# Kernel tuning notes

Measured on AMD Instinct MI355X. Metric: run time of the kernel, lower is better.

Reference implementation:

```python
import jax, jax.numpy as jnp
import numpy as np

B, S, C, H, E, K = 8, 512, 768, 12, 8, 2
MLP_H = int(C * 4.0)
HD = C // H
ROUTER_REG = 0.01
LN_EPS = 1e-5


def setup_inputs() -> dict:
    key = jax.random.key(0)
    ks = jax.random.split(key, 8)

    def w(k, shape, fan_in):
        return (jax.random.normal(k, shape, dtype=jnp.float32) / np.sqrt(fan_in)).astype(jnp.float32)

    return {
        "x": jax.random.normal(ks[0], (B, S, C), dtype=jnp.float32),
        "expert_tokens": w(ks[1], (E, C), C),
        "ln1_g": jnp.ones((E, C), jnp.float32),
        "ln1_b": jnp.zeros((E, C), jnp.float32),
        "qkv_w": w(ks[2], (E, C, 3 * C), C),
        "qkv_b": jnp.zeros((E, 3 * C), jnp.float32),
        "proj_w": w(ks[3], (E, C, C), C),
        "proj_b": jnp.zeros((E, C), jnp.float32),
        "ln2_g": jnp.ones((E, C), jnp.float32),
        "ln2_b": jnp.zeros((E, C), jnp.float32),
        "fc1_w": w(ks[4], (E, C, MLP_H), C),
        "fc1_b": jnp.zeros((E, MLP_H), jnp.float32),
        "fc2_w": w(ks[5], (E, MLP_H, C), MLP_H),
        "fc2_b": jnp.zeros((E, C), jnp.float32),
    }


def _layernorm(x, g, b):
    mu = jnp.mean(x, axis=-1, keepdims=True)
    var = jnp.mean(jnp.square(x - mu), axis=-1, keepdims=True)
    return (x - mu) * jax.lax.rsqrt(var + LN_EPS) * g + b


def _block(x, p):
    # One transformer Block (pre-LN attention + MLP), params for a single expert.
    ln1_g, ln1_b, qkv_w, qkv_b, proj_w, proj_b, ln2_g, ln2_b, fc1_w, fc1_b, fc2_w, fc2_b = p
    h = _layernorm(x, ln1_g, ln1_b)
    qkv = (h @ qkv_w + qkv_b).reshape(B, S, 3, H, HD)
    q, k, v = qkv[:, :, 0], qkv[:, :, 1], qkv[:, :, 2]  # [B,S,H,HD]
    # NOTE: original code MULTIPLIES by sqrt(head_dim) (scale = head_dim**0.5).
    scale = jnp.float32(np.sqrt(HD))
    attn = jax.nn.softmax(jnp.einsum('bqhd,bkhd->bhqk', q, k) * scale, axis=-1)
    o = jnp.einsum('bhqk,bkhd->bqhd', attn, v).reshape(B, S, C)
    x = x + (o @ proj_w + proj_b)
    h2 = _layernorm(x, ln2_g, ln2_b)
    x = x + (jax.nn.gelu(h2 @ fc1_w + fc1_b, approximate=False) @ fc2_w + fc2_b)
    return x


def reference(x, expert_tokens, ln1_g, ln1_b, qkv_w, qkv_b, proj_w, proj_b,
              ln2_g, ln2_b, fc1_w, fc1_b, fc2_w, fc2_b):
    # Router
    router_logits = jnp.einsum('bsc,nc->bsn', x, expert_tokens) / jnp.float32(np.sqrt(C))
    router_probs = jax.nn.softmax(router_logits, axis=-1)
    top_k_probs, top_k_idx = jax.lax.top_k(router_probs, K)  # [B,S,K]
    top_k_probs = top_k_probs / jnp.sum(top_k_probs, axis=-1, keepdims=True)

    # Dense all-expert compute (sequential over experts to bound memory)
    params = (ln1_g, ln1_b, qkv_w, qkv_b, proj_w, proj_b, ln2_g, ln2_b,
              fc1_w, fc1_b, fc2_w, fc2_b)
    expert_out = jax.lax.map(lambda p: _block(x, p), params)  # [E,B,S,C]
    expert_out = jnp.transpose(expert_out, (1, 2, 0, 3))       # [B,S,E,C]

    # Top-k gather and weighted combine
    sel = jnp.take_along_axis(expert_out, top_k_idx[..., None], axis=2)  # [B,S,K,C]
    combine = jnp.sum(sel * top_k_probs[..., None], axis=2)
    out = x + combine

    # Load-balance auxiliary loss
    counts = jnp.sum(jax.nn.one_hot(top_k_idx, E, dtype=jnp.float32), axis=(0, 1, 2))
    f_i = counts / jnp.float32(B * S * K)
    P_i = jnp.mean(router_probs, axis=(0, 1))
    balance_loss = E * jnp.sum(f_i * P_i) + ROUTER_REG * jnp.linalg.norm(expert_tokens)
    return out, balance_loss
```

## Files before the change

### kernel.cpp

```cpp
#include <hip/hip_runtime.h>
#include <hip/hip_bf16.h>

#define BB 8
#define SS 512
#define CC 768
#define HH 12
#define HD 64
#define EE 8
#define KK 2
#define MLPH 3072
#define NT (BB*SS)
#define NOUT (NT*CC)

#define SLOTB      68059136ull
#define SLOT_U16   34029568ull
#define SLOT_F32   17014784ull

typedef unsigned int u32;
typedef unsigned short u16;
typedef __attribute__((ext_vector_type(8))) short short8;
typedef __attribute__((ext_vector_type(4))) float f32x4;

__device__ __forceinline__ u16 f2bf(float f) {
    u32 u = __builtin_bit_cast(u32, f);
    u32 r = (u + 0x7fffu + ((u >> 16) & 1u)) >> 16;
    return (u16)r;
}
__device__ __forceinline__ float bf2f(u16 h) {
    u32 u = ((u32)h) << 16;
    return __builtin_bit_cast(float, u);
}
__device__ __forceinline__ void gl_lds16(const void* g, void* l) {
    __builtin_amdgcn_global_load_lds(
        (const __attribute__((address_space(1))) u32*)g,
        (__attribute__((address_space(3))) u32*)l, 16, 0, 0);
}
__device__ __forceinline__ void swz_rc(int bid, int& bm, int& bn) {
    int xcd = bid & 7, off = bid >> 3;
    bm = (xcd * 4 + (off & 3)) * 128;
    bn = (off >> 2) * 128;
}

__device__ __forceinline__ void stage128x64(const u16* __restrict__ G, size_t ldg,
                                            u16* s, int tid)
{
    int wid = tid >> 6, lane = tid & 63;
#pragma unroll
    for (int it = 0; it < 4; ++it) {
        int cb = it * 256 + wid * 64;
        int c = cb + lane;
        int row = c >> 3;
        int ch = (c & 7) ^ (row & 7);
        gl_lds16(G + (size_t)row * ldg + ch * 8, s + cb * 8);
    }
}
__device__ __forceinline__ short8 frag64(const u16* s, int row, int kc, int lb) {
    int ch = (kc * 4 + lb) ^ (row & 7);
    return *(const short8*)(s + row * 64 + ch * 8);
}

__global__ __launch_bounds__(256) void router_kernel(const float* __restrict__ x,
    const float* __restrict__ et, float* __restrict__ W, float* __restrict__ stats)
{
    __shared__ float etl[EE * CC];
    __shared__ float pred[4][2 * EE];
    int tid = threadIdx.x;
    for (int i = tid; i < EE * CC; i += 256) etl[i] = et[i];
    __syncthreads();
    int wid = tid >> 6, lane = tid & 63;
    float psum[EE] = {}, csum[EE] = {};
    for (int i = 0; i < 2; i++) {
        int t = blockIdx.x * 8 + wid * 2 + i;
        const float* xr = x + (size_t)t * CC;
        float acc[EE] = {};
        for (int c = lane; c < CC; c += 64) {
            float xv = xr[c];
#pragma unroll
            for (int e = 0; e < EE; e++) acc[e] += xv * etl[e * CC + c];
        }
#pragma unroll
        for (int e = 0; e < EE; e++)
            for (int off = 1; off < 64; off <<= 1) acc[e] += __shfl_xor(acc[e], off, 64);
        if (lane == 0) {
            const float inv = 0.03608439182435161f;
            float l[EE], m = -1e30f;
#pragma unroll
            for (int e = 0; e < EE; e++) { l[e] = acc[e] * inv; m = fmaxf(m, l[e]); }
            float p[EE], sum = 0.f;
#pragma unroll
            for (int e = 0; e < EE; e++) { p[e] = __expf(l[e] - m); sum += p[e]; }
            int i1 = 0;
#pragma unroll
            for (int e = 1; e < EE; e++) if (p[e] > p[i1]) i1 = e;
            int i2 = -1;
#pragma unroll
            for (int e = 0; e < EE; e++) if (e != i1 && (i2 < 0 || p[e] > p[i2])) i2 = e;
            float wn = p[i1] + p[i2];
#pragma unroll
            for (int e = 0; e < EE; e++) W[t * EE + e] = 0.f;
            W[t * EE + i1] = p[i1] / wn;
            W[t * EE + i2] = p[i2] / wn;
#pragma unroll
            for (int e = 0; e < EE; e++) psum[e] += p[e] / sum;
            csum[i1] += 1.f; csum[i2] += 1.f;
        }
    }
    if (lane == 0) {
#pragma unroll
        for (int e = 0; e < EE; e++) { pred[wid][e] = psum[e]; pred[wid][EE + e] = csum[e]; }
    }
    __syncthreads();
    if (tid < 2 * EE) {
        float s = pred[0][tid] + pred[1][tid] + pred[2][tid] + pred[3][tid];
        atomicAdd(&stats[tid], s);
    }
}

template<int MODE>
__global__ __launch_bounds__(256) void ln_kernel(const float* __restrict__ x, size_t xslot,
    u16* __restrict__ out_hi, u16* __restrict__ out_lo, size_t oslot)
{
    int t = blockIdx.x;
    int eb = blockIdx.y;
    const float* xr = x + (size_t)eb * xslot + (size_t)t * CC;
    __shared__ float red[256];
    int tid = threadIdx.x;
    float v[3];
    float s = 0.f;
#pragma unroll
    for (int i = 0; i < 3; i++) { v[i] = xr[tid + i * 256]; s += v[i]; }
    red[tid] = s; __syncthreads();
    for (int off = 128; off > 0; off >>= 1) { if (tid < off) red[tid] += red[tid + off]; __syncthreads(); }
    float mu = red[0] / (float)CC;
    __syncthreads();
    float s2 = 0.f;
#pragma unroll
    for (int i = 0; i < 3; i++) { float d = v[i] - mu; s2 += d * d; }
    red[tid] = s2; __syncthreads();
    for (int off = 128; off > 0; off >>= 1) { if (tid < off) red[tid] += red[tid + off]; __syncthreads(); }
    float var = red[0] / (float)CC;
    float sc = rsqrtf(var + 1e-5f);
#pragma unroll
    for (int i = 0; i < 3; i++) {
        int c = tid + i * 256;
        float val = (v[i] - mu) * sc;
        u16 hi = f2bf(val);
        out_hi[(size_t)eb * oslot + (size_t)t * CC + c] = hi;
        if (MODE) out_lo[(size_t)eb * oslot + (size_t)t * CC + c] = f2bf(val - bf2f(hi));
    }
}

__global__ __launch_bounds__(256) void prep_expert(
    const float* __restrict__ qkv_w0, const float* __restrict__ qkv_b0,
    const float* __restrict__ proj_w0,
    const float* __restrict__ fc1_w0, const float* __restrict__ fc1_b0,
    const float* __restrict__ fc2_w0,
    const float* __restrict__ g1_0, const float* __restrict__ b1_0,
    const float* __restrict__ g2_0, const float* __restrict__ b2_0,
    u16* __restrict__ qkvTh, u16* __restrict__ qkvTl,
    u16* __restrict__ projT, u16* __restrict__ fc1T, u16* __restrict__ fc2T,
    float* __restrict__ biasq, float* __restrict__ biasf1, int ebase)
{
    __shared__ float tile[32][33];
    __shared__ float bsh[CC];
    __shared__ float redg[256];
    int bid = blockIdx.x;
    int eb = blockIdx.y;
    int ge = ebase + eb;
    int tid = threadIdx.x;
    const float* qkv_w = qkv_w0 + (size_t)ge * CC * 3 * CC;
    const float* qkv_b = qkv_b0 + (size_t)ge * 3 * CC;
    const float* proj_w = proj_w0 + (size_t)ge * CC * CC;
    const float* fc1_w = fc1_w0 + (size_t)ge * CC * MLPH;
    const float* fc1_b = fc1_b0 + (size_t)ge * MLPH;
    const float* fc2_w = fc2_w0 + (size_t)ge * MLPH * CC;
    const float* g1 = g1_0 + (size_t)ge * CC;
    const float* b1 = b1_0 + (size_t)ge * CC;
    const float* g2 = g2_0 + (size_t)ge * CC;
    const float* b2 = b2_0 + (size_t)ge * CC;

    if (bid < 6912) {
        const float* src; const float* scale = nullptr;
        u16 *dh, *dl = nullptr; int N, Kd, n0, k0;
        if (bid < 1728) {
            src = qkv_w; scale = g1;
            dh = qkvTh + (size_t)eb * SLOT_U16; dl = qkvTl + (size_t)eb * SLOT_U16;
            N = 2304; Kd = 768; n0 = (bid % 72) * 32; k0 = (bid / 72) * 32;
        } else if (bid < 2304) {
            int i = bid - 1728;
            src = proj_w; dh = projT + (size_t)eb * SLOT_U16; N = 768; Kd = 768;
            n0 = (i % 24) * 32; k0 = (i / 24) * 32;
        } else if (bid < 4608) {
            int i = bid - 2304;
            src = fc1_w; scale = g2; dh = fc1T + (size_t)eb * SLOT_U16; N = 3072; Kd = 768;
            n0 = (i % 96) * 32; k0 = (i / 96) * 32;
        } else {
            int i = bid - 4608;
            src = fc2_w; dh = fc2T + (size_t)eb * SLOT_U16; N = 768; Kd = 3072;
            n0 = (i % 24) * 32; k0 = (i / 24) * 32;
        }
        int tx = tid & 31, ty = tid >> 5;
#pragma unroll
        for (int i = 0; i < 32; i += 8) {
            float v = src[(size_t)(k0 + ty + i) * N + n0 + tx];
            if (scale) v *= scale[k0 + ty + i];
            tile[ty + i][tx] = v;
        }
        __syncthreads();
#pragma unroll
        for (int i = 0; i < 32; i += 8) {
            float v = tile[tx][ty + i];
            u16 hi = f2bf(v);
            dh[(size_t)(n0 + ty + i) * Kd + k0 + tx] = hi;
            if (dl) dl[(size_t)(n0 + ty + i) * Kd + k0 + tx] = f2bf(v - bf2f(hi));
        }
    } else {
        const float* bv; const float* wsrc; const float* badd;
        float* dst; int N, n0;
        if (bid < 6984) { bv = b1; wsrc = qkv_w; badd = qkv_b; dst = biasq + (size_t)eb * SLOT_F32; N = 2304; n0 = (bid - 6912) * 32; }
        else            { bv = b2; wsrc = fc1_w; badd = fc1_b; dst = biasf1 + (size_t)eb * SLOT_F32; N = MLPH; n0 = (bid - 6984) * 32; }
        for (int i = tid; i < CC; i += 256) bsh[i] = bv[i];
        __syncthreads();
        int g = tid & 31, l8 = tid >> 5;
        int n = n0 + g;
        float acc = 0.f;
        for (int k = l8; k < CC; k += 8) acc += bsh[k] * wsrc[(size_t)k * N + n];
        redg[tid] = acc; __syncthreads();
        if (tid < 32) {
            float sum = 0.f;
#pragma unroll
            for (int i = 0; i < 8; i++) sum += redg[tid + i * 32];
            dst[n0 + tid] = sum + badd[n0 + tid];
        }
    }
}

__global__ __launch_bounds__(256) void gemm_qkv_bk64(
    const u16* __restrict__ Ah, const u16* __restrict__ Al,
    const u16* __restrict__ Bh0, const u16* __restrict__ Bl0,
    const float* __restrict__ biasq0, u16* __restrict__ qk_hi0,
    u16* __restrict__ qk_lo0, u16* __restrict__ vtout0)
{
    __shared__ __align__(16) u16 sAh[128 * 64], sAl[128 * 64];
    __shared__ __align__(16) u16 sBh[128 * 64], sBl[128 * 64];
    int tid = threadIdx.x;
    int eb = blockIdx.y;
    int bm, bn;
    swz_rc(blockIdx.x, bm, bn);
    bool qk_tile = (bn < 1536);
    int wid = tid >> 6, lane = tid & 63;
    int wr = wid >> 1, wc = wid & 1;
    int la = lane & 15, lb = lane >> 4;
    const u16* Bh = Bh0 + (size_t)eb * SLOT_U16;
    const u16* Bl = Bl0 + (size_t)eb * SLOT_U16;
    const float* bias = biasq0 + (size_t)eb * SLOT_F32;
    u16* qk_hi = qk_hi0 + (size_t)eb * SLOT_U16;
    u16* qk_lo = qk_lo0 + (size_t)eb * SLOT_U16;
    u16* vtout = vtout0 + (size_t)eb * SLOT_U16;

    f32x4 acc[4][4];
#pragma unroll
    for (int i = 0; i < 4; i++)
#pragma unroll
        for (int j = 0; j < 4; j++) acc[i][j] = (f32x4){0.f, 0.f, 0.f, 0.f};

    const u16* Abh = Ah + (size_t)bm * CC;
    const u16* Abl = Al + (size_t)bm * CC;
    const u16* Bbh = Bh + (size_t)bn * CC;
    const u16* Bbl = Bl + (size_t)bn * CC;
    for (int k0 = 0; k0 < CC; k0 += 64) {
        stage128x64(Abh + k0, CC, sAh, tid);
        stage128x64(Bbh + k0, CC, sBh, tid);
        if (qk_tile) {
            stage128x64(Abl + k0, CC, sAl, tid);
            stage128x64(Bbl + k0, CC, sBl, tid);
        }
        __syncthreads();
        if (qk_tile) {
#pragma unroll
            for (int kc = 0; kc < 2; kc++) {
                short8 avh[4], avl[4], bvh[4], bvl[4];
#pragma unroll
                for (int i = 0; i < 4; i++) {
                    int row = wr * 64 + i * 16 + la;
                    avh[i] = frag64(sAh, row, kc, lb);
                    avl[i] = frag64(sAl, row, kc, lb);
                }
#pragma unroll
                for (int j = 0; j < 4; j++) {
                    int row = wc * 64 + j * 16 + la;
                    bvh[j] = frag64(sBh, row, kc, lb);
                    bvl[j] = frag64(sBl, row, kc, lb);
                }
#pragma unroll
                for (int i = 0; i < 4; i++)
#pragma unroll
                    for (int j = 0; j < 4; j++) {
                        acc[i][j] = __builtin_amdgcn_mfma_f32_16x16x32_bf16(avh[i], bvh[j], acc[i][j], 0, 0, 0);
                        acc[i][j] = __builtin_amdgcn_mfma_f32_16x16x32_bf16(avh[i], bvl[j], acc[i][j], 0, 0, 0);
                        acc[i][j] = __builtin_amdgcn_mfma_f32_16x16x32_bf16(avl[i], bvh[j], acc[i][j], 0, 0, 0);
                    }
            }
        } else {
#pragma unroll
            for (int kc = 0; kc < 2; kc++) {
                short8 avh[4], bvh[4];
#pragma unroll
                for (int i = 0; i < 4; i++) avh[i] = frag64(sAh, wr * 64 + i * 16 + la, kc, lb);
#pragma unroll
                for (int j = 0; j < 4; j++) bvh[j] = frag64(sBh, wc * 64 + j * 16 + la, kc, lb);
#pragma unroll
                for (int i = 0; i < 4; i++)
#pragma unroll
                    for (int j = 0; j < 4; j++)
                        acc[i][j] = __builtin_amdgcn_mfma_f32_16x16x32_bf16(avh[i], bvh[j], acc[i][j], 0, 0, 0);
            }
        }
        __syncthreads();
    }
#pragma unroll
    for (int i = 0; i < 4; i++) {
#pragma unroll
        for (int j = 0; j < 4; j++) {
            int gn = bn + wc * 64 + j * 16 + la;
            float bsv = bias[gn];
#pragma unroll
            for (int r = 0; r < 4; r++) {
                int gm = bm + wr * 64 + i * 16 + lb * 4 + r;
                float v = acc[i][j][r] + bsv;
                if (gn < 1536) {
                    u16 hi = f2bf(v);
                    qk_hi[(size_t)gm * 1536 + gn] = hi;
                    qk_lo[(size_t)gm * 1536 + gn] = f2bf(v - bf2f(hi));
                } else {
                    int dd = (gn - 1536) & 63, hh = (gn - 1536) >> 6;
                    int ss = gm & (SS - 1), bb = gm >> 9;
                    vtout[((size_t)((bb * HH + hh) * HD + dd)) * SS + ss] = f2bf(v);
                }
            }
        }
    }
}

template<int EPI>
__global__ __launch_bounds__(256) void gemm_b(
    const u16* __restrict__ A, size_t Aslot,
    const u16* __restrict__ BT, size_t Bslot,
    const float* __restrict__ bias, size_t biasSlot,
    const float* __restrict__ res, size_t resSlot,
    const float* __restrict__ Wt, int ebase,
    const float* __restrict__ xinit,
    void* __restrict__ Cout, size_t CoutSlot, int N, int Kdim)
{
    __shared__ __align__(16) u16 sA[128 * 64];
    __shared__ __align__(16) u16 sB[128 * 64];
    int tid = threadIdx.x;
    int eb = blockIdx.y;
    int ge = ebase + eb;
    int bm, bn;
    swz_rc(blockIdx.x, bm, bn);
    int wid = tid >> 6, lane = tid & 63;
    int wr = wid >> 1, wc = wid & 1;
    int la = lane & 15, lb = lane >> 4;
    f32x4 acc[4][4];
#pragma unroll
    for (int i = 0; i < 4; i++)
#pragma unroll
        for (int j = 0; j < 4; j++) acc[i][j] = (f32x4){0.f, 0.f, 0.f, 0.f};

    const u16* Ab = A + (size_t)eb * Aslot + (size_t)bm * Kdim;
    const u16* Bb = BT + (size_t)eb * Bslot + (size_t)bn * Kdim;
    for (int k0 = 0; k0 < Kdim; k0 += 64) {
        stage128x64(Ab + k0, Kdim, sA, tid);
        stage128x64(Bb + k0, Kdim, sB, tid);
        __syncthreads();
#pragma unroll
        for (int kc = 0; kc < 2; kc++) {
            short8 av[4], bv[4];
#pragma unroll
            for (int i = 0; i < 4; i++) av[i] = frag64(sA, wr * 64 + i * 16 + la, kc, lb);
#pragma unroll
            for (int j = 0; j < 4; j++) bv[j] = frag64(sB, wc * 64 + j * 16 + la, kc, lb);
#pragma unroll
            for (int i = 0; i < 4; i++)
#pragma unroll
                for (int j = 0; j < 4; j++)
                    acc[i][j] = __builtin_amdgcn_mfma_f32_16x16x32_bf16(av[i], bv[j], acc[i][j], 0, 0, 0);
        }
        __syncthreads();
    }
    const float* biasp = bias + (size_t)eb * biasSlot;
    const float* resp = res ? res + (size_t)eb * resSlot : nullptr;
#pragma unroll
    for (int i = 0; i < 4; i++) {
#pragma unroll
        for (int j = 0; j < 4; j++) {
            int gn = bn + wc * 64 + j * 16 + la;
            float bsv = biasp[gn];
#pragma unroll
            for (int r = 0; r < 4; r++) {
                int gm = bm + wr * 64 + i * 16 + lb * 4 + r;
                size_t idx = (size_t)gm * N + gn;
                float v = acc[i][j][r];
                if (EPI == 1) {
                    ((float*)Cout + (size_t)eb * CoutSlot)[idx] = resp[idx] + v + bsv;
                } else {
                    float w = Wt[(size_t)gm * EE + ge];
                    float val = w * (v + bsv + resp[idx]);
                    if (ge == 0) val += xinit[idx];
                    atomicAdd(&((float*)Cout)[idx], val);
                }
            }
        }
    }
}

__global__ __launch_bounds__(512, 2) void gemm_fc1_p(
    const u16* __restrict__ A0, const u16* __restrict__ BT0,
    const float* __restrict__ bias0, u16* __restrict__ C0)
{
    __shared__ __align__(16) u16 sA[3][256 * 32];
    __shared__ __align__(16) u16 sB[3][256 * 32];
    const int NTILE = CC / 32;
    int tid = threadIdx.x;
    int eb = blockIdx.y;
    int xcd = blockIdx.x & 7, off = blockIdx.x >> 3;
    int lid = xcd * 24 + off;
    int bn = (lid / 16) * 256;
    int bm = (lid % 16) * 256;
    int wid = tid >> 6, lane = tid & 63;
    int wm = wid >> 2, wn = wid & 3;
    int la = lane & 15, lb = lane >> 4;

    const u16* Ab = A0 + (size_t)eb * SLOT_U16 + (size_t)bm * CC;
    const u16* Bb = BT0 + (size_t)eb * SLOT_U16 + (size_t)bn * CC;

    auto STG = [&](int s, int t) {
#pragma unroll
        for (int rd = 0; rd < 2; rd++) {
            int cb = rd * 512 + wid * 64;
            int c = cb + lane;
            gl_lds16(Ab + (size_t)(c >> 2) * CC + t * 32 + (c & 3) * 8, &sA[s][(size_t)cb * 8]);
        }
#pragma unroll
        for (int rd = 0; rd < 2; rd++) {
            int cb = rd * 512 + wid * 64;
            int c = cb + lane;
            gl_lds16(Bb + (size_t)(c >> 2) * CC + t * 32 + (c & 3) * 8, &sB[s][(size_t)cb * 8]);
        }
    };

    f32x4 acc[8][4];
#pragma unroll
    for (int i = 0; i < 8; i++)
#pragma unroll
        for (int j = 0; j < 4; j++) acc[i][j] = (f32x4){0.f, 0.f, 0.f, 0.f};

    STG(0, 0);
    STG(1, 1);

    for (int t = 0; t < NTILE; t++) {
        if (t < NTILE - 1) asm volatile("s_waitcnt vmcnt(4)" ::: "memory");
        else               asm volatile("s_waitcnt vmcnt(0)" ::: "memory");
        asm volatile("" ::: "memory");
        __builtin_amdgcn_s_barrier();
        asm volatile("" ::: "memory");

        const u16* cA = &sA[t % 3][0];
        const u16* cB = &sB[t % 3][0];
        __builtin_amdgcn_s_setprio(1);
        short8 bfr[4];
#pragma unroll
        for (int j = 0; j < 4; j++)
            bfr[j] = *(const short8*)(cB + ((size_t)(wn * 64 + j * 16 + la) * 4 + lb) * 8);
#pragma unroll
        for (int i = 0; i < 8; i++) {
            short8 af = *(const short8*)(cA + ((size_t)(wm * 128 + i * 16 + la) * 4 + lb) * 8);
#pragma unroll
            for (int j = 0; j < 4; j++)
                acc[i][j] = __builtin_amdgcn_mfma_f32_16x16x32_bf16(af, bfr[j], acc[i][j], 0, 0, 0);
        }
        __builtin_amdgcn_s_setprio(0);

        if (t + 2 < NTILE) STG((t + 2) % 3, t + 2);
    }

    const float* bp = bias0 + (size_t)eb * SLOT_F32;
    u16* C = C0 + (size_t)eb * SLOT_U16;
#pragma unroll
    for (int i = 0; i < 8; i++) {
#pragma unroll
        for (int j = 0; j < 4; j++) {
            int gn = bn + wn * 64 + j * 16 + la;
            float bsv = bp[gn];
#pragma unroll
            for (int r = 0; r < 4; r++) {
                int gm = bm + wm * 128 + i * 16 + lb * 4 + r;
                float v = acc[i][j][r] + bsv;
                float gel = 0.5f * v * (1.0f + erff(v * 0.70710678118654752f));
                C[(size_t)gm * MLPH + gn] = f2bf(gel);
            }
        }
    }
}

__global__ __launch_bounds__(256) void attn_mfma(const u16* __restrict__ qk_hi0,
    const u16* __restrict__ qk_lo0, const u16* __restrict__ vt0, u16* __restrict__ o0)
{
    int q0 = blockIdx.x * 64;
    int h = blockIdx.y;
    int z = blockIdx.z;
    int b = z & (BB - 1), eb = z >> 3;
    int tid = threadIdx.x, wid = tid >> 6, lane = tid & 63;
    int la = lane & 15, lb = lane >> 4;
    __shared__ __align__(16) u16 Ksh[64 * 64];
    __shared__ __align__(16) u16 Ksl[64 * 64];
    __shared__ __align__(16) u16 Vs[64 * 64];
    __shared__ __align__(16) u16 Ps[4][16 * 64];

    const u16* qk_hi = qk_hi0 + (size_t)eb * SLOT_U16;
    const u16* qk_lo = qk_lo0 + (size_t)eb * SLOT_U16;
    const u16* vt = vt0 + (size_t)eb * SLOT_U16;
    u16* o = o0 + (size_t)eb * SLOT_U16;

    short8 aqh[2], aql[2];
    {
        size_t qoff = (size_t)(b * SS + q0 + wid * 16 + la) * 1536 + h * HD;
#pragma unroll
        for (int kc = 0; kc < 2; kc++) {
            aqh[kc] = *(const short8*)(qk_hi + qoff + kc * 32 + lb * 8);
            aql[kc] = *(const short8*)(qk_lo + qoff + kc * 32 + lb * 8);
        }
    }
    const u16* kbh = qk_hi + (size_t)(b * SS) * 1536 + CC + h * HD;
    const u16* kbl = qk_lo + (size_t)(b * SS) * 1536 + CC + h * HD;
    const u16* vtbase = vt + (size_t)((b * HH + h) * HD) * SS;

    float m_r[4], l_r[4];
    f32x4 acc_o[4];
#pragma unroll
    for (int r = 0; r < 4; r++) { m_r[r] = -1e30f; l_r[r] = 0.f; }
#pragma unroll
    for (int d0 = 0; d0 < 4; d0++) acc_o[d0] = (f32x4){0.f, 0.f, 0.f, 0.f};

    for (int kt = 0; kt < SS; kt += 64) {
#pragma unroll
        for (int it = 0; it < 2; it++) {
            int base = it * 256 + wid * 64;
            int c = base + lane;
            int row = c >> 3;
            int gk = (c & 7) ^ (row & 7);
            gl_lds16(kbh + (size_t)(kt + row) * 1536 + gk * 8, Ksh + base * 8);
            gl_lds16(kbl + (size_t)(kt + row) * 1536 + gk * 8, Ksl + base * 8);
            gl_lds16(vtbase + (size_t)row * SS + kt + gk * 8, Vs + base * 8);
        }
        __syncthreads();

        f32x4 s4[4];
#pragma unroll
        for (int j = 0; j < 4; j++) s4[j] = (f32x4){0.f, 0.f, 0.f, 0.f};
#pragma unroll
        for (int kc = 0; kc < 2; kc++)
#pragma unroll
            for (int j = 0; j < 4; j++) {
                size_t off = (size_t)(j * 16 + la) * 64 + (((kc * 4 + lb) ^ (la & 7)) * 8);
                short8 bkh = *(const short8*)(Ksh + off);
                short8 bkl = *(const short8*)(Ksl + off);
                s4[j] = __builtin_amdgcn_mfma_f32_16x16x32_bf16(aqh[kc], bkh, s4[j], 0, 0, 0);
                s4[j] = __builtin_amdgcn_mfma_f32_16x16x32_bf16(aql[kc], bkh, s4[j], 0, 0, 0);
                s4[j] = __builtin_amdgcn_mfma_f32_16x16x32_bf16(aqh[kc], bkl, s4[j], 0, 0, 0);
            }
#pragma unroll
        for (int j = 0; j < 4; j++) s4[j] = s4[j] * 8.f;

#pragma unroll
        for (int r = 0; r < 4; r++) {
            float mx = fmaxf(fmaxf(s4[0][r], s4[1][r]), fmaxf(s4[2][r], s4[3][r]));
#pragma unroll
            for (int off = 1; off < 16; off <<= 1) mx = fmaxf(mx, __shfl_xor(mx, off, 64));
            float mn = fmaxf(m_r[r], mx);
            float corr = __expf(m_r[r] - mn);
            m_r[r] = mn;
            float rs = 0.f;
#pragma unroll
            for (int j = 0; j < 4; j++) {
                float p = __expf(s4[j][r] - mn);
                s4[j][r] = p; rs += p;
            }
#pragma unroll
            for (int off = 1; off < 16; off <<= 1) rs += __shfl_xor(rs, off, 64);
            l_r[r] = l_r[r] * corr + rs;
#pragma unroll
            for (int d0 = 0; d0 < 4; d0++) acc_o[d0][r] = acc_o[d0][r] * corr;
        }
#pragma unroll
        for (int j = 0; j < 4; j++)
#pragma unroll
            for (int r = 0; r < 4; r++) {
                int row = lb * 4 + r;
                int sg = (2 * j + (la >> 3)) ^ (row & 7);
                Ps[wid][row * 64 + sg * 8 + (la & 7)] = f2bf(s4[j][r]);
            }
        short8 pa[2];
#pragma unroll
        for (int kc = 0; kc < 2; kc++)
            pa[kc] = *(const short8*)(&Ps[wid][la * 64 + (((kc * 4 + lb) ^ (la & 7)) * 8)]);
#pragma unroll
        for (int d0 = 0; d0 < 4; d0++)
#pragma unroll
            for (int kc = 0; kc < 2; kc++) {
                short8 bv = *(const short8*)(&Vs[(d0 * 16 + la) * 64 + (((kc * 4 + lb) ^ (la & 7)) * 8)]);
                acc_o[d0] = __builtin_amdgcn_mfma_f32_16x16x32_bf16(pa[kc], bv, acc_o[d0], 0, 0, 0);
            }
        __syncthreads();
    }
#pragma unroll
    for (int r = 0; r < 4; r++) {
        float invl = 1.f / l_r[r];
        int tok = b * SS + q0 + wid * 16 + lb * 4 + r;
#pragma unroll
        for (int d0 = 0; d0 < 4; d0++)
            o[(size_t)tok * CC + h * HD + d0 * 16 + la] = f2bf(acc_o[d0][r] * invl);
    }
}

__global__ __launch_bounds__(256) void loss_kernel(const float* __restrict__ et,
    const float* __restrict__ stats, float* __restrict__ out_loss)
{
    __shared__ float red[256];
    int tid = threadIdx.x;
    float s = 0.f;
    for (int i = tid; i < EE * CC; i += 256) { float v = et[i]; s += v * v; }
    red[tid] = s; __syncthreads();
    for (int off = 128; off > 0; off >>= 1) { if (tid < off) red[tid] += red[tid + off]; __syncthreads(); }
    if (tid == 0) {
        float bl = 0.f;
        for (int e = 0; e < EE; e++) {
            float f = stats[EE + e] / (float)(NT * KK);
            float P = stats[e] / (float)NT;
            bl += f * P;
        }
        *out_loss = (float)EE * bl + 0.01f * sqrtf(red[0]);
    }
}

extern "C" void kernel_launch(void* const* d_in, const int* in_sizes, int n_in,
                              void* d_out, int out_size, void* d_ws, size_t ws_size,
                              hipStream_t stream) {
    const float* x      = (const float*)d_in[0];
    const float* et     = (const float*)d_in[1];
    const float* ln1_g  = (const float*)d_in[2];
    const float* ln1_b  = (const float*)d_in[3];
    const float* qkv_w  = (const float*)d_in[4];
    const float* qkv_b  = (const float*)d_in[5];
    const float* proj_w = (const float*)d_in[6];
    const float* proj_b = (const float*)d_in[7];
    const float* ln2_g  = (const float*)d_in[8];
    const float* ln2_b  = (const float*)d_in[9];
    const float* fc1_w  = (const float*)d_in[10];
    const float* fc1_b  = (const float*)d_in[11];
    const float* fc2_w  = (const float*)d_in[12];
    const float* fc2_b  = (const float*)d_in[13];
    float* outp = (float*)d_out;
    char* base = (char*)d_ws;

    const size_t FIXED = 12714496;
    int EB = 1;
    if (ws_size >= FIXED + 8 * SLOTB) EB = 8;
    else if (ws_size >= FIXED + 4 * SLOTB) EB = 4;
    else if (ws_size >= FIXED + 2 * SLOTB) EB = 2;

    float* W      = (float*)(base);
    float* stats  = (float*)(base + 131072);
    u16*   xh_hi  = (u16*)  (base + 131584);
    u16*   xh_lo  = (u16*)  (base + 6423040);
    char* slot0 = base + FIXED;
    u16*   qkvTh  = (u16*)  (slot0);
    u16*   qkvTl  = (u16*)  (slot0 + 3538944);
    u16*   projT  = (u16*)  (slot0 + 7077888);
    u16*   fc1T   = (u16*)  (slot0 + 8257536);
    u16*   fc2T   = (u16*)  (slot0 + 12976128);
    float* biasq  = (float*)(slot0 + 17694720);
    float* biasf1 = (float*)(slot0 + 17711104);
    u16*   qk_hi  = (u16*)  (slot0 + 17727488);
    u16*   qk_lo  = (u16*)  (slot0 + 30310400);
    u16*   mlp1   = (u16*)  (slot0 + 17727488);
    u16*   vtb    = (u16*)  (slot0 + 42893312);
    u16*   xmhat  = (u16*)  (slot0 + 42893312);
    u16*   obf    = (u16*)  (slot0 + 49184768);
    float* xmid   = (float*)(slot0 + 55476224);

    hipMemsetAsync(stats, 0, 16 * sizeof(float), stream);
    hipMemsetAsync(outp, 0, (size_t)NOUT * sizeof(float), stream);

    router_kernel<<<NT / 8, 256, 0, stream>>>(x, et, W, stats);
    ln_kernel<1><<<dim3(NT, 1), 256, 0, stream>>>(x, 0, xh_hi, xh_lo, 0);

    for (int ebase = 0; ebase < EE; ebase += EB) {
        prep_expert<<<dim3(7080, EB), 256, 0, stream>>>(
            qkv_w, qkv_b, proj_w, fc1_w, fc1_b, fc2_w,
            ln1_g, ln1_b, ln2_g, ln2_b,
            qkvTh, qkvTl, projT, fc1T, fc2T, biasq, biasf1, ebase);

        gemm_qkv_bk64<<<dim3(18 * 32, EB), 256, 0, stream>>>(
            xh_hi, xh_lo, qkvTh, qkvTl, biasq, qk_hi, qk_lo, vtb);

        attn_mfma<<<dim3(SS / 64, HH, BB * EB), 256, 0, stream>>>(qk_hi, qk_lo, vtb, obf);

        gemm_b<1><<<dim3(6 * 32, EB), 256, 0, stream>>>(
            obf, SLOT_U16, projT, SLOT_U16, proj_b + (size_t)ebase * CC, CC,
            x, 0, nullptr, 0, nullptr, xmid, SLOT_F32, CC, CC);

        ln_kernel<0><<<dim3(NT, EB), 256, 0, stream>>>(xmid, SLOT_F32, xmhat, nullptr, SLOT_U16);

        gemm_fc1_p<<<dim3(192, EB), 512, 0, stream>>>(xmhat, fc1T, biasf1, mlp1);

        gemm_b<5><<<dim3(6 * 32, EB), 256, 0, stream>>>(
            mlp1, SLOT_U16, fc2T, SLOT_U16, fc2_b + (size_t)ebase * CC, CC,
            xmid, SLOT_F32, W, ebase, x, outp, 0, CC, MLPH);
    }

    loss_kernel<<<1, 256, 0, stream>>>(et, stats, outp + NOUT);
}
```

Measured before the change: 1.598 ms.

## Unify fc1/fc2 GEMMs on triple-buffered 128x128 direct-to-LDS pipeline

The fc2 GEMM moves from the synchronous 64-wide-K staging loop to the triple-buffered, waitcnt-pipelined BK=32 body that fc1 used. fc1 shrinks from 256x256 tiles with 512 threads to 128x128 tiles with 256 threads, with a shared body for both. The proj GEMM is specialised into its own kernel with constants baked in. The aim is to hide global-load latency in fc2's long K=3072 loop and raise occupancy and tile count for fc1, at the cost of less data reuse per fc1 tile. The fc2 epilogue no longer adds the bias inside the weighted term separately from v; it is folded into v, which is equivalent.

```diff
diff --git a/kernel.cpp b/kernel.cpp
--- a/kernel.cpp
+++ b/kernel.cpp
@@ -57,6 +57,24 @@
 __device__ __forceinline__ short8 frag64(const u16* s, int row, int kc, int lb) {
     int ch = (kc * 4 + lb) ^ (row & 7);
     return *(const short8*)(s + row * 64 + ch * 8);
+}
+
+__device__ __forceinline__ void stg_dp(const u16* __restrict__ A, const u16* __restrict__ B,
+                                       int ldk, u16* sA, u16* sB, int t, int tid)
+{
+    int wid = tid >> 6, lane = tid & 63;
+#pragma unroll
+    for (int rd = 0; rd < 2; rd++) {
+        int cb = rd * 256 + wid * 64;
+        int c = cb + lane;
+        gl_lds16(A + (size_t)(c >> 2) * ldk + t * 32 + (c & 3) * 8, sA + cb * 8);
+    }
+#pragma unroll
+    for (int rd = 0; rd < 2; rd++) {
+        int cb = rd * 256 + wid * 64;
+        int c = cb + lane;
+        gl_lds16(B + (size_t)(c >> 2) * ldk + t * 32 + (c & 3) * 8, sB + cb * 8);
+    }
 }
 
 __global__ __launch_bounds__(256) void router_kernel(const float* __restrict__ x,
@@ -342,21 +360,15 @@
     }
 }
 
-template<int EPI>
-__global__ __launch_bounds__(256) void gemm_b(
-    const u16* __restrict__ A, size_t Aslot,
-    const u16* __restrict__ BT, size_t Bslot,
-    const float* __restrict__ bias, size_t biasSlot,
-    const float* __restrict__ res, size_t resSlot,
-    const float* __restrict__ Wt, int ebase,
-    const float* __restrict__ xinit,
-    void* __restrict__ Cout, size_t CoutSlot, int N, int Kdim)
+__global__ __launch_bounds__(256) void gemm_proj(
+    const u16* __restrict__ A, const u16* __restrict__ BT,
+    const float* __restrict__ bias0, const float* __restrict__ x,
+    float* __restrict__ Cout)
 {
     __shared__ __align__(16) u16 sA[128 * 64];
     __shared__ __align__(16) u16 sB[128 * 64];
     int tid = threadIdx.x;
     int eb = blockIdx.y;
-    int ge = ebase + eb;
     int bm, bn;
     swz_rc(blockIdx.x, bm, bn);
     int wid = tid >> 6, lane = tid & 63;
@@ -368,11 +380,11 @@
 #pragma unroll
         for (int j = 0; j < 4; j++) acc[i][j] = (f32x4){0.f, 0.f, 0.f, 0.f};
 
-    const u16* Ab = A + (size_t)eb * Aslot + (size_t)bm * Kdim;
-    const u16* Bb = BT + (size_t)eb * Bslot + (size_t)bn * Kdim;
-    for (int k0 = 0; k0 < Kdim; k0 += 64) {
-        stage128x64(Ab + k0, Kdim, sA, tid);
-        stage128x64(Bb + k0, Kdim, sB, tid);
+    const u16* Ab = A + (size_t)eb * SLOT_U16 + (size_t)bm * CC;
+    const u16* Bb = BT + (size_t)eb * SLOT_U16 + (size_t)bn * CC;
+    for (int k0 = 0; k0 < CC; k0 += 64) {
+        stage128x64(Ab + k0, CC, sA, tid);
+        stage128x64(Bb + k0, CC, sB, tid);
         __syncthreads();
 #pragma unroll
         for (int kc = 0; kc < 2; kc++) {
@@ -389,8 +401,8 @@
         }
         __syncthreads();
     }
-    const float* biasp = bias + (size_t)eb * biasSlot;
-    const float* resp = res ? res + (size_t)eb * resSlot : nullptr;
+    const float* biasp = bias0 + (size_t)eb * CC;
+    float* C = Cout + (size_t)eb * SLOT_F32;
 #pragma unroll
     for (int i = 0; i < 4; i++) {
 #pragma unroll
@@ -400,64 +412,36 @@
 #pragma unroll
             for (int r = 0; r < 4; r++) {
                 int gm = bm + wr * 64 + i * 16 + lb * 4 + r;
-                size_t idx = (size_t)gm * N + gn;
-                float v = acc[i][j][r];
-                if (EPI == 1) {
-                    ((float*)Cout + (size_t)eb * CoutSlot)[idx] = resp[idx] + v + bsv;
-                } else {
-                    float w = Wt[(size_t)gm * EE + ge];
-                    float val = w * (v + bsv + resp[idx]);
-                    if (ge == 0) val += xinit[idx];
-                    atomicAdd(&((float*)Cout)[idx], val);
-                }
-            }
-        }
-    }
-}
-
-__global__ __launch_bounds__(512, 2) void gemm_fc1_p(
-    const u16* __restrict__ A0, const u16* __restrict__ BT0,
-    const float* __restrict__ bias0, u16* __restrict__ C0)
-{
-    __shared__ __align__(16) u16 sA[3][256 * 32];
-    __shared__ __align__(16) u16 sB[3][256 * 32];
-    const int NTILE = CC / 32;
+                size_t idx = (size_t)gm * CC + gn;
+                C[idx] = x[idx] + acc[i][j][r] + bsv;
+            }
+        }
+    }
+}
+
+template<int EPI>
+__device__ __forceinline__ void gemm_dp_body(
+    const u16* __restrict__ Ab, const u16* __restrict__ Bb, int Kdim,
+    const float* __restrict__ biasp, const float* __restrict__ resp,
+    const float* __restrict__ Wt, int ge, const float* __restrict__ xinit,
+    void* __restrict__ Cout, int N, int bm, int bn)
+{
+    __shared__ __align__(16) u16 sA[3][128 * 32];
+    __shared__ __align__(16) u16 sB[3][128 * 32];
     int tid = threadIdx.x;
-    int eb = blockIdx.y;
-    int xcd = blockIdx.x & 7, off = blockIdx.x >> 3;
-    int lid = xcd * 24 + off;
-    int bn = (lid / 16) * 256;
-    int bm = (lid % 16) * 256;
     int wid = tid >> 6, lane = tid & 63;
-    int wm = wid >> 2, wn = wid & 3;
+    int wr = wid >> 1, wc = wid & 1;
     int la = lane & 15, lb = lane >> 4;
-
-    const u16* Ab = A0 + (size_t)eb * SLOT_U16 + (size_t)bm * CC;
-    const u16* Bb = BT0 + (size_t)eb * SLOT_U16 + (size_t)bn * CC;
-
-    auto STG = [&](int s, int t) {
-#pragma unroll
-        for (int rd = 0; rd < 2; rd++) {
-            int cb = rd * 512 + wid * 64;
-            int c = cb + lane;
-            gl_lds16(Ab + (size_t)(c >> 2) * CC + t * 32 + (c & 3) * 8, &sA[s][(size_t)cb * 8]);
-        }
-#pragma unroll
-        for (int rd = 0; rd < 2; rd++) {
-            int cb = rd * 512 + wid * 64;
-            int c = cb + lane;
-            gl_lds16(Bb + (size_t)(c >> 2) * CC + t * 32 + (c & 3) * 8, &sB[s][(size_t)cb * 8]);
-        }
-    };
-
-    f32x4 acc[8][4];
-#pragma unroll
-    for (int i = 0; i < 8; i++)
+    int NTILE = Kdim / 32;
+
+    f32x4 acc[4][4];
+#pragma unroll
+    for (int i = 0; i < 4; i++)
 #pragma unroll
         for (int j = 0; j < 4; j++) acc[i][j] = (f32x4){0.f, 0.f, 0.f, 0.f};
 
-    STG(0, 0);
-    STG(1, 1);
+    stg_dp(Ab, Bb, Kdim, sA[0], sB[0], 0, tid);
+    stg_dp(Ab, Bb, Kdim, sA[1], sB[1], 1, tid);
 
     for (int t = 0; t < NTILE; t++) {
         if (t < NTILE - 1) asm volatile("s_waitcnt vmcnt(4)" ::: "memory");
@@ -469,39 +453,73 @@
         const u16* cA = &sA[t % 3][0];
         const u16* cB = &sB[t % 3][0];
         __builtin_amdgcn_s_setprio(1);
-        short8 bfr[4];
+        short8 bv[4];
 #pragma unroll
         for (int j = 0; j < 4; j++)
-            bfr[j] = *(const short8*)(cB + ((size_t)(wn * 64 + j * 16 + la) * 4 + lb) * 8);
-#pragma unroll
-        for (int i = 0; i < 8; i++) {
-            short8 af = *(const short8*)(cA + ((size_t)(wm * 128 + i * 16 + la) * 4 + lb) * 8);
+            bv[j] = *(const short8*)(cB + ((size_t)(wc * 64 + j * 16 + la) * 4 + lb) * 8);
+#pragma unroll
+        for (int i = 0; i < 4; i++) {
+            short8 av = *(const short8*)(cA + ((size_t)(wr * 64 + i * 16 + la) * 4 + lb) * 8);
 #pragma unroll
             for (int j = 0; j < 4; j++)
-                acc[i][j] = __builtin_amdgcn_mfma_f32_16x16x32_bf16(af, bfr[j], acc[i][j], 0, 0, 0);
+                acc[i][j] = __builtin_amdgcn_mfma_f32_16x16x32_bf16(av, bv[j], acc[i][j], 0, 0, 0);
         }
         __builtin_amdgcn_s_setprio(0);
 
-        if (t + 2 < NTILE) STG((t + 2) % 3, t + 2);
-    }
-
-    const float* bp = bias0 + (size_t)eb * SLOT_F32;
-    u16* C = C0 + (size_t)eb * SLOT_U16;
-#pragma unroll
-    for (int i = 0; i < 8; i++) {
+        if (t + 2 < NTILE) stg_dp(Ab, Bb, Kdim, sA[(t + 2) % 3], sB[(t + 2) % 3], t + 2, tid);
+    }
+
+#pragma unroll
+    for (int i = 0; i < 4; i++) {
 #pragma unroll
         for (int j = 0; j < 4; j++) {
-            int gn = bn + wn * 64 + j * 16 + la;
-            float bsv = bp[gn];
+            int gn = bn + wc * 64 + j * 16 + la;
+            float bsv = biasp[gn];
 #pragma unroll
             for (int r = 0; r < 4; r++) {
-                int gm = bm + wm * 128 + i * 16 + lb * 4 + r;
+                int gm = bm + wr * 64 + i * 16 + lb * 4 + r;
+                size_t idx = (size_t)gm * N + gn;
                 float v = acc[i][j][r] + bsv;
-                float gel = 0.5f * v * (1.0f + erff(v * 0.70710678118654752f));
-                C[(size_t)gm * MLPH + gn] = f2bf(gel);
-            }
-        }
-    }
+                if (EPI == 2) {
+                    float gel = 0.5f * v * (1.0f + erff(v * 0.70710678118654752f));
+                    ((u16*)Cout)[idx] = f2bf(gel);
+                } else {
+                    float w = Wt[(size_t)gm * EE + ge];
+                    float val = w * (v + resp[idx]);
+                    if (ge == 0) val += xinit[idx];
+                    atomicAdd(&((float*)Cout)[idx], val);
+                }
+            }
+        }
+    }
+}
+
+__global__ __launch_bounds__(256) void gemm_fc1_dp(
+    const u16* __restrict__ A0, const u16* __restrict__ BT0,
+    const float* __restrict__ bias0, u16* __restrict__ C0)
+{
+    int eb = blockIdx.y;
+    int bm, bn;
+    swz_rc(blockIdx.x, bm, bn);
+    gemm_dp_body<2>(A0 + (size_t)eb * SLOT_U16 + (size_t)bm * CC,
+                    BT0 + (size_t)eb * SLOT_U16 + (size_t)bn * CC, CC,
+                    bias0 + (size_t)eb * SLOT_F32, nullptr, nullptr, 0, nullptr,
+                    C0 + (size_t)eb * SLOT_U16, MLPH, bm, bn);
+}
+
+__global__ __launch_bounds__(256) void gemm_fc2_dp(
+    const u16* __restrict__ A0, const u16* __restrict__ BT0,
+    const float* __restrict__ bias0, const float* __restrict__ res0,
+    const float* __restrict__ Wt, int ebase, const float* __restrict__ xinit,
+    float* __restrict__ Cout)
+{
+    int eb = blockIdx.y;
+    int bm, bn;
+    swz_rc(blockIdx.x, bm, bn);
+    gemm_dp_body<5>(A0 + (size_t)eb * SLOT_U16 + (size_t)bm * MLPH,
+                    BT0 + (size_t)eb * SLOT_U16 + (size_t)bn * MLPH, MLPH,
+                    bias0 + (size_t)eb * CC, res0 + (size_t)eb * SLOT_F32,
+                    Wt, ebase + eb, xinit, Cout, CC, bm, bn);
 }
 
 __global__ __launch_bounds__(256) void attn_mfma(const u16* __restrict__ qk_hi0,
@@ -707,17 +725,15 @@
 
         attn_mfma<<<dim3(SS / 64, HH, BB * EB), 256, 0, stream>>>(qk_hi, qk_lo, vtb, obf);
 
-        gemm_b<1><<<dim3(6 * 32, EB), 256, 0, stream>>>(
-            obf, SLOT_U16, projT, SLOT_U16, proj_b + (size_t)ebase * CC, CC,
-            x, 0, nullptr, 0, nullptr, xmid, SLOT_F32, CC, CC);
+        gemm_proj<<<dim3(6 * 32, EB), 256, 0, stream>>>(
+            obf, projT, proj_b + (size_t)ebase * CC, x, xmid);
 
         ln_kernel<0><<<dim3(NT, EB), 256, 0, stream>>>(xmid, SLOT_F32, xmhat, nullptr, SLOT_U16);
 
-        gemm_fc1_p<<<dim3(192, EB), 512, 0, stream>>>(xmhat, fc1T, biasf1, mlp1);
-
-        gemm_b<5><<<dim3(6 * 32, EB), 256, 0, stream>>>(
-            mlp1, SLOT_U16, fc2T, SLOT_U16, fc2_b + (size_t)ebase * CC, CC,
-            xmid, SLOT_F32, W, ebase, x, outp, 0, CC, MLPH);
+        gemm_fc1_dp<<<dim3(24 * 32, EB), 256, 0, stream>>>(xmhat, fc1T, biasf1, mlp1);
+
+        gemm_fc2_dp<<<dim3(6 * 32, EB), 256, 0, stream>>>(
+            mlp1, fc2T, fc2_b + (size_t)ebase * CC, xmid, W, ebase, x, outp);
     }
 
     loss_kernel<<<1, 256, 0, stream>>>(et, stats, outp + NOUT);
```

Result: faster. 1.448 ms (-9.4%).
